# Performance work log

Hardware: AMD Instinct MI355X
Metric: run time of the kernel (lower is better)

The kernel has to match this reference:

```python
import jax, jax.numpy as jnp
import numpy as np

N_GRAPHS = 100
BN_EPS = 1e-5
L = 4


def batch_norm(x, gamma, beta):
    # torch BatchNorm1d in training mode: biased batch statistics over the node dim
    mu = jnp.mean(x, axis=0)
    var = jnp.var(x, axis=0)
    return gamma * (x - mu) * jax.lax.rsqrt(var + BN_EPS) + beta


def setup_inputs() -> dict:
    key = jax.random.key(0)
    ks = jax.random.split(key, 24)
    N, E, IN, H, C = 50000, 600000, 128, 128, 10
    s = 0.05
    inp = {
        "h": jax.random.normal(ks[0], (N, IN), jnp.float32),
        "snorm_n": jax.random.uniform(ks[1], (N, 1), jnp.float32),
        "edge_src": jax.random.randint(ks[2], (E,), 0, N, jnp.int32),
        "edge_dst": jax.random.randint(ks[3], (E,), 0, N, jnp.int32),
        "graph_ids": jnp.sort(jax.random.randint(ks[4], (N,), 0, N_GRAPHS, jnp.int32)),
        # embedding_h
        "emb_W": jax.random.normal(ks[5], (IN, H), jnp.float32) * s,
        "emb_b": jnp.zeros((H,), jnp.float32),
        # per-layer GIN params, stacked over L layers
        "eps": jnp.zeros((L,), jnp.float32),
        "W1": jax.random.normal(ks[6], (L, H, H), jnp.float32) * s,
        "b1": jnp.zeros((L, H), jnp.float32),
        "g1": jnp.ones((L, H), jnp.float32),   # MLP internal BN gamma
        "be1": jnp.zeros((L, H), jnp.float32),  # MLP internal BN beta
        "W2": jax.random.normal(ks[7], (L, H, H), jnp.float32) * s,
        "b2": jnp.zeros((L, H), jnp.float32),
        "ga": jnp.ones((L, H), jnp.float32),    # ApplyNodeFunc BN gamma
        "ba": jnp.zeros((L, H), jnp.float32),
        "gl": jnp.ones((L, H), jnp.float32),    # GINLayer node BN gamma
        "bl": jnp.zeros((L, H), jnp.float32),
        # linears_prediction (L+1 of them)
        "pred_W": jax.random.normal(ks[8], (L + 1, H, C), jnp.float32) * s,
        "pred_b": jnp.zeros((L + 1, C), jnp.float32),
    }
    return inp


def reference(h, snorm_n, edge_src, edge_dst, graph_ids, emb_W, emb_b, eps,
              W1, b1, g1, be1, W2, b2, ga, ba, gl, bl, pred_W, pred_b):
    N = h.shape[0]
    h = h @ emb_W + emb_b  # embedding_h
    hidden_rep = [h]
    for i in range(L):
        h_in = h
        # sum-aggregate neighbor features (irregular gather + scatter-add)
        neigh = jax.ops.segment_sum(h[edge_src], edge_dst, num_segments=N)
        z = (1.0 + eps[i]) * h + neigh
        # ApplyNodeFunc: MLP (lin->BN->relu->lin) then BN then relu
        z = jax.nn.relu(batch_norm(z @ W1[i] + b1[i], g1[i], be1[i]))
        z = z @ W2[i] + b2[i]
        z = jax.nn.relu(batch_norm(z, ga[i], ba[i]))
        z = z * snorm_n                      # graph_norm
        z = batch_norm(z, gl[i], bl[i])      # batch_norm
        z = jax.nn.relu(z)
        h = h_in + z                         # residual (dropout p=0)
        hidden_rep.append(h)
    score = jnp.zeros((N_GRAPHS, pred_W.shape[-1]), h.dtype)
    for i, hr in enumerate(hidden_rep):
        pooled = jax.ops.segment_sum(hr, graph_ids, num_segments=N_GRAPHS)
        score = score + pooled @ pred_W[i] + pred_b[i]
    return score
```

## Files before the change

### kernel.cpp

```cpp
#include <hip/hip_runtime.h>

#define HD __device__ __forceinline__

static constexpr int H = 128;
static constexpr int G = 100;
static constexpr int L = 4;
static constexpr int C = 10;
static constexpr int DEGCAP = 64;

typedef __attribute__((ext_vector_type(8))) short short8;
typedef __attribute__((ext_vector_type(4))) float f32x4;

HD float bf2f(unsigned int u16) {
    return __uint_as_float(u16 << 16);
}
HD unsigned int f2bf(float f) {
    unsigned int u = __float_as_uint(f);
    u += 0x7fffu + ((u >> 16) & 1u);
    return u >> 16;
}

__global__ __launch_bounds__(256) void prep_kernel(
    const float* __restrict__ embW, const float* __restrict__ W1, const float* __restrict__ W2,
    unsigned short* __restrict__ WT, unsigned short* __restrict__ Hb,
    const int* __restrict__ src, const int* __restrict__ dst, int E,
    int* __restrict__ cnt, int* __restrict__ esrc) {
    int b = blockIdx.x;
    if (b < 576) {
        int mat = b >> 6;
        int bx = b & 63;
        if (b == 0 && threadIdx.x < 64)
            ((unsigned int*)Hb)[threadIdx.x] = 0u;
        const float* s = (mat == 0) ? embW
                       : (mat <= L) ? W1 + (size_t)(mat - 1) * H * H
                                    : W2 + (size_t)(mat - 1 - L) * H * H;
        int t = bx * 256 + threadIdx.x;
        int col = t >> 7, k = t & 127;
        WT[(size_t)mat * H * H + col * H + k] = (unsigned short)f2bf(s[(size_t)k * H + col]);
    } else {
        int e = (b - 576) * 256 + threadIdx.x;
        if (e < E) {
            int d = dst[e];
            int pos = atomicAdd(&cnt[d], 1) & (DEGCAP - 1);
            esrc[(size_t)d * DEGCAP + pos] = src[e] + 1;
        }
    }
}

__global__ __launch_bounds__(1024, 2) void aggemm_kernel(
    const unsigned short* __restrict__ HbZ, const int* __restrict__ cnt,
    const int* __restrict__ esrc, const float* __restrict__ eps, int layer,
    const unsigned short* __restrict__ WT, const float* __restrict__ bias,
    unsigned short* __restrict__ outB, int N,
    float* __restrict__ sum_out, float* __restrict__ sq_out) {
    __shared__ unsigned short As[64 * 136];
    int tid = threadIdx.x;
    int w = tid >> 6, lane = tid & 63, q = lane >> 4, m = lane & 15;
    int row0 = blockIdx.x * 64;

    {
        const unsigned int* H2 = (const unsigned int*)HbZ;
        float e1 = 1.0f + eps[layer];
#pragma unroll
        for (int i = 0; i < 4; ++i) {
            int r = w * 4 + i;
            int node = row0 + r;
            unsigned int out = 0;
            if (node < N) {
                unsigned int hv = H2[(size_t)(node + 1) * 64 + lane];
                float ax = e1 * bf2f(hv & 0xffffu);
                float ay = e1 * bf2f(hv >> 16);
                int deg = min(cnt[node], DEGCAP);
                int degPad = min((deg + 15) & ~15, DEGCAP);
                const int* ep = esrc + (size_t)node * DEGCAP;
                for (int j = 0; j < degPad; j += 16) {
                    unsigned int v[16];
#pragma unroll
                    for (int u = 0; u < 16; ++u) v[u] = H2[(size_t)ep[j + u] * 64 + lane];
                    float sx[4] = {0.f, 0.f, 0.f, 0.f}, sy[4] = {0.f, 0.f, 0.f, 0.f};
#pragma unroll
                    for (int u = 0; u < 16; ++u) {
                        sx[u & 3] += bf2f(v[u] & 0xffffu);
                        sy[u & 3] += bf2f(v[u] >> 16);
                    }
                    ax += (sx[0] + sx[1]) + (sx[2] + sx[3]);
                    ay += (sy[0] + sy[1]) + (sy[2] + sy[3]);
                }
                out = f2bf(ax) | (f2bf(ay) << 16);
            }
            *(unsigned int*)&As[r * 136 + lane * 2] = out;
        }
    }
    __syncthreads();

    int mrow = (w >> 2) * 16;
    int colbase = (w & 3) * 32;
    short8 bfrag[2][4];
#pragma unroll
    for (int nt = 0; nt < 2; ++nt) {
        const unsigned short* wc = WT + (size_t)(colbase + nt * 16 + m) * H;
#pragma unroll
        for (int kk = 0; kk < 4; ++kk)
            bfrag[nt][kk] = *(const short8*)&wc[kk * 32 + q * 8];
    }
    f32x4 acc[2] = {(f32x4){0.f, 0.f, 0.f, 0.f}, (f32x4){0.f, 0.f, 0.f, 0.f}};
#pragma unroll
    for (int kk = 0; kk < 4; ++kk) {
        short8 af = *(const short8*)&As[(mrow + m) * 136 + kk * 32 + q * 8];
#pragma unroll
        for (int nt = 0; nt < 2; ++nt)
            acc[nt] = __builtin_amdgcn_mfma_f32_16x16x32_bf16(af, bfrag[nt][kk], acc[nt], 0, 0, 0);
    }

    float bs2[2] = {bias[colbase + m], bias[colbase + 16 + m]};
    float s[2] = {0.f, 0.f}, qq[2] = {0.f, 0.f};
#pragma unroll
    for (int nt = 0; nt < 2; ++nt) {
        int gcol = colbase + nt * 16 + m;
#pragma unroll
        for (int rg = 0; rg < 4; ++rg) {
            int grow = row0 + mrow + q * 4 + rg;
            float v = acc[nt][rg] + bs2[nt];
            if (grow < N) {
                outB[(size_t)grow * H + gcol] = (unsigned short)f2bf(v);
                s[nt] += v;
                qq[nt] += v * v;
            }
        }
    }
#pragma unroll
    for (int nt = 0; nt < 2; ++nt) {
        s[nt] += __shfl_xor(s[nt], 16); s[nt] += __shfl_xor(s[nt], 32);
        qq[nt] += __shfl_xor(qq[nt], 16); qq[nt] += __shfl_xor(qq[nt], 32);
    }
    __syncthreads();
    float* SS = (float*)As;
    float* QQ = SS + 4 * H;
    if (q == 0) {
#pragma unroll
        for (int nt = 0; nt < 2; ++nt) {
            int col = colbase + nt * 16 + m;
            SS[(w >> 2) * H + col] = s[nt];
            QQ[(w >> 2) * H + col] = qq[nt];
        }
    }
    __syncthreads();
    if (tid < H) {
        atomicAdd(&sum_out[tid], SS[tid] + SS[H + tid] + SS[2 * H + tid] + SS[3 * H + tid]);
        atomicAdd(&sq_out[tid], QQ[tid] + QQ[H + tid] + QQ[2 * H + tid] + QQ[3 * H + tid]);
    }
}

template <bool ABF16, bool TRANS, bool STATS, bool POOLF, bool HOFF>
__global__ __launch_bounds__(256, 4) void mgemm_kernel(
    const float* __restrict__ Af, const unsigned short* __restrict__ Ab,
    const unsigned short* __restrict__ WT, const float* __restrict__ bias,
    const float* __restrict__ sum_in, const float* __restrict__ sq_in,
    const float* __restrict__ gam, const float* __restrict__ bet, float invN,
    unsigned short* __restrict__ outB,
    int N, float* __restrict__ sum_out, float* __restrict__ sq_out,
    const int* __restrict__ gids, float* __restrict__ pool) {
    __shared__ unsigned short As[64 * 136];
    __shared__ float cas[H], ccs[H];
    int tid = threadIdx.x;
    int w = tid >> 6, lane = tid & 63, q = lane >> 4, m = lane & 15;
    int row0 = blockIdx.x * 64;
    int colbase = w * 32;

    short8 bfrag[2][4];
#pragma unroll
    for (int nt = 0; nt < 2; ++nt) {
        const unsigned short* wc = WT + (size_t)(colbase + nt * 16 + m) * H;
#pragma unroll
        for (int kk = 0; kk < 4; ++kk)
            bfrag[nt][kk] = *(const short8*)&wc[kk * 32 + q * 8];
    }

    if (TRANS) {
        if (tid < H) {
            float mu = sum_in[tid] * invN;
            float var = sq_in[tid] * invN - mu * mu;
            float inv = rsqrtf(var + 1e-5f);
            float a = gam[tid] * inv;
            cas[tid] = a;
            ccs[tid] = bet[tid] - mu * a;
        }
        __syncthreads();
    }

    {
        int cc = tid & 15, rg = tid >> 4;
        int c0 = cc * 8;
        float a8[8], b8[8];
        if (TRANS) {
#pragma unroll
            for (int j = 0; j < 8; ++j) { a8[j] = cas[c0 + j]; b8[j] = ccs[c0 + j]; }
        }
#pragma unroll
        for (int rr = 0; rr < 4; ++rr) {
            int r = rg * 4 + rr;
            int gr = row0 + r;
            uint4 o = {0u, 0u, 0u, 0u};
            if (ABF16 && !TRANS) {
                if (gr < N) o = *(const uint4*)&Ab[(size_t)gr * H + c0];
            } else {
                float v[8] = {0.f, 0.f, 0.f, 0.f, 0.f, 0.f, 0.f, 0.f};
                if (gr < N) {
                    if (ABF16) {
                        uint4 x = *(const uint4*)&Ab[(size_t)gr * H + c0];
                        v[0] = bf2f(x.x & 0xffffu); v[1] = bf2f(x.x >> 16);
                        v[2] = bf2f(x.y & 0xffffu); v[3] = bf2f(x.y >> 16);
                        v[4] = bf2f(x.z & 0xffffu); v[5] = bf2f(x.z >> 16);
                        v[6] = bf2f(x.w & 0xffffu); v[7] = bf2f(x.w >> 16);
                    } else {
                        float4 x0 = *(const float4*)&Af[(size_t)gr * H + c0];
                        float4 x1 = *(const float4*)&Af[(size_t)gr * H + c0 + 4];
                        v[0] = x0.x; v[1] = x0.y; v[2] = x0.z; v[3] = x0.w;
                        v[4] = x1.x; v[5] = x1.y; v[6] = x1.z; v[7] = x1.w;
                    }
                }
                if (TRANS) {
#pragma unroll
                    for (int j = 0; j < 8; ++j) v[j] = fmaxf(a8[j] * v[j] + b8[j], 0.f);
                }
                o.x = f2bf(v[0]) | (f2bf(v[1]) << 16);
                o.y = f2bf(v[2]) | (f2bf(v[3]) << 16);
                o.z = f2bf(v[4]) | (f2bf(v[5]) << 16);
                o.w = f2bf(v[6]) | (f2bf(v[7]) << 16);
            }
            *(uint4*)&As[r * 136 + c0] = o;
        }
    }
    __syncthreads();

    f32x4 acc[4][2];
#pragma unroll
    for (int mt = 0; mt < 4; ++mt)
#pragma unroll
        for (int nt = 0; nt < 2; ++nt) acc[mt][nt] = (f32x4){0.f, 0.f, 0.f, 0.f};
#pragma unroll
    for (int kk = 0; kk < 4; ++kk) {
        short8 af[4];
#pragma unroll
        for (int mt = 0; mt < 4; ++mt)
            af[mt] = *(const short8*)&As[(mt * 16 + m) * 136 + kk * 32 + q * 8];
#pragma unroll
        for (int mt = 0; mt < 4; ++mt)
#pragma unroll
            for (int nt = 0; nt < 2; ++nt)
                acc[mt][nt] = __builtin_amdgcn_mfma_f32_16x16x32_bf16(
                    af[mt], bfrag[nt][kk], acc[mt][nt], 0, 0, 0);
    }

    float bs2[2] = {bias[colbase + m], bias[colbase + 16 + m]};
    float s[2] = {0.f, 0.f}, qq[2] = {0.f, 0.f};
#pragma unroll
    for (int mt = 0; mt < 4; ++mt)
#pragma unroll
        for (int nt = 0; nt < 2; ++nt) {
            int gcol = colbase + nt * 16 + m;
#pragma unroll
            for (int rg = 0; rg < 4; ++rg) {
                int grow = row0 + mt * 16 + q * 4 + rg;
                float v = acc[mt][nt][rg] + bs2[nt];
                if (grow < N) {
                    outB[(size_t)(HOFF ? grow + 1 : grow) * H + gcol] = (unsigned short)f2bf(v);
                    if (STATS || POOLF) {
                        s[nt] += v;
                        if (STATS) qq[nt] += v * v;
                    }
                }
            }
        }

    if (STATS) {
#pragma unroll
        for (int nt = 0; nt < 2; ++nt) {
            float sv = s[nt], qv = qq[nt];
            sv += __shfl_xor(sv, 16); sv += __shfl_xor(sv, 32);
            qv += __shfl_xor(qv, 16); qv += __shfl_xor(qv, 32);
            if (q == 0) {
                atomicAdd(&sum_out[colbase + nt * 16 + m], sv);
                atomicAdd(&sq_out[colbase + nt * 16 + m], qv);
            }
        }
    }

    if (POOLF) {
        int last = min(row0 + 63, N - 1);
        bool uni = (gids[row0] == gids[last]);
        if (uni) {
            int g = gids[row0];
#pragma unroll
            for (int nt = 0; nt < 2; ++nt) {
                float sv = s[nt];
                sv += __shfl_xor(sv, 16); sv += __shfl_xor(sv, 32);
                if (q == 0) atomicAdd(&pool[g * H + colbase + nt * 16 + m], sv);
            }
        } else {
#pragma unroll
            for (int mt = 0; mt < 4; ++mt)
#pragma unroll
                for (int nt = 0; nt < 2; ++nt)
#pragma unroll
                    for (int rg = 0; rg < 4; ++rg) {
                        int grow = row0 + mt * 16 + q * 4 + rg;
                        if (grow < N) {
                            float v = acc[mt][nt][rg] + bs2[nt];
                            atomicAdd(&pool[gids[grow] * H + colbase + nt * 16 + m], v);
                        }
                    }
        }
    }
}

__global__ __launch_bounds__(256) void statsv_kernel(const unsigned short* __restrict__ UB,
                                                     const float* __restrict__ snorm,
                                                     const float* __restrict__ sum2, const float* __restrict__ sq2,
                                                     const float* __restrict__ ga, const float* __restrict__ ba,
                                                     float invN, int N,
                                                     float* __restrict__ sum3, float* __restrict__ sq3) {
    __shared__ float cas[H], ccs[H];
    int t = threadIdx.x;
    if (t < H) {
        float m = sum2[t] * invN;
        float var = sq2[t] * invN - m * m;
        float inv = rsqrtf(var + 1e-5f);
        float a = ga[t] * inv;
        cas[t] = a;
        ccs[t] = ba[t] - m * a;
    }
    __syncthreads();
    int col2 = t & 63, part = t >> 6;
    int c0 = col2 * 2, c1 = c0 + 1;
    float a0 = cas[c0], b0 = ccs[c0], a1 = cas[c1], b1 = ccs[c1];
    float s0 = 0.f, q0 = 0.f, s1 = 0.f, q1 = 0.f;
    const unsigned int* U2 = (const unsigned int*)UB;
    for (int r = blockIdx.x * 4 + part; r < N; r += gridDim.x * 4) {
        float sn = snorm[r];
        unsigned int v = U2[(size_t)r * 64 + col2];
        float v0 = fmaxf(a0 * bf2f(v & 0xffffu) + b0, 0.f) * sn;
        float v1 = fmaxf(a1 * bf2f(v >> 16) + b1, 0.f) * sn;
        s0 += v0; q0 += v0 * v0;
        s1 += v1; q1 += v1 * v1;
    }
    __shared__ float S[4][H], Q[4][H];
    S[part][c0] = s0; S[part][c1] = s1;
    Q[part][c0] = q0; Q[part][c1] = q1;
    __syncthreads();
    if (t < H) {
        atomicAdd(&sum3[t], S[0][t] + S[1][t] + S[2][t] + S[3][t]);
        atomicAdd(&sq3[t], Q[0][t] + Q[1][t] + Q[2][t] + Q[3][t]);
    }
}

__global__ __launch_bounds__(256) void tail_kernel(unsigned short* __restrict__ HbZ,
                                                   const unsigned short* __restrict__ UB,
                                                   const float* __restrict__ snorm,
                                                   const float* __restrict__ sum2, const float* __restrict__ sq2,
                                                   const float* __restrict__ ga, const float* __restrict__ ba,
                                                   const float* __restrict__ sum3, const float* __restrict__ sq3,
                                                   const float* __restrict__ gl, const float* __restrict__ bl,
                                                   float invN, const int* __restrict__ gids,
                                                   float* __restrict__ pool, int N) {
    __shared__ float ca2[H], cc2[H], ca3[H], cc3[H];
    __shared__ float PS[8][H];
    int t = threadIdx.x;
    if (t < H) {
        float m2 = sum2[t] * invN, v2 = sq2[t] * invN - m2 * m2;
        float i2 = rsqrtf(v2 + 1e-5f), a2 = ga[t] * i2;
        ca2[t] = a2; cc2[t] = ba[t] - m2 * a2;
        float m3 = sum3[t] * invN, v3 = sq3[t] * invN - m3 * m3;
        float i3 = rsqrtf(v3 + 1e-5f), a3 = gl[t] * i3;
        ca3[t] = a3; cc3[t] = bl[t] - m3 * a3;
    }
    __syncthreads();
    int row0 = blockIdx.x * 32;
    int col4 = t & 31, rowg = t >> 5;
    int c0 = col4 * 4;
    float A2[4], B2[4], A3[4], B3[4];
#pragma unroll
    for (int j = 0; j < 4; ++j) {
        A2[j] = ca2[c0 + j]; B2[j] = cc2[c0 + j];
        A3[j] = ca3[c0 + j]; B3[j] = cc3[c0 + j];
    }
    bool uni = (gids[row0] == gids[min(row0 + 31, N - 1)]);
    float p[4] = {0.f, 0.f, 0.f, 0.f};
    const uint2* U4 = (const uint2*)UB;
    uint2* H4 = (uint2*)HbZ;
#pragma unroll
    for (int rr = 0; rr < 4; ++rr) {
        int r = row0 + rowg * 4 + rr;
        if (r < N) {
            float sn = snorm[r];
            uint2 uv = U4[(size_t)r * 32 + col4];
            uint2 hv = H4[(size_t)(r + 1) * 32 + col4];
            float u[4] = {bf2f(uv.x & 0xffffu), bf2f(uv.x >> 16), bf2f(uv.y & 0xffffu), bf2f(uv.y >> 16)};
            float h[4] = {bf2f(hv.x & 0xffffu), bf2f(hv.x >> 16), bf2f(hv.y & 0xffffu), bf2f(hv.y >> 16)};
#pragma unroll
            for (int j = 0; j < 4; ++j) {
                float v = fmaxf(A2[j] * u[j] + B2[j], 0.f) * sn;
                h[j] += fmaxf(A3[j] * v + B3[j], 0.f);
            }
            uint2 hb;
            hb.x = f2bf(h[0]) | (f2bf(h[1]) << 16);
            hb.y = f2bf(h[2]) | (f2bf(h[3]) << 16);
            H4[(size_t)(r + 1) * 32 + col4] = hb;
            if (uni) {
                p[0] += h[0]; p[1] += h[1]; p[2] += h[2]; p[3] += h[3];
            } else {
                int g = gids[r];
#pragma unroll
                for (int j = 0; j < 4; ++j) atomicAdd(&pool[g * H + c0 + j], h[j]);
            }
        }
    }
    if (uni) {
#pragma unroll
        for (int j = 0; j < 4; ++j) PS[rowg][c0 + j] = p[j];
        __syncthreads();
        if (t < H) {
            float s = PS[0][t] + PS[1][t] + PS[2][t] + PS[3][t] +
                      PS[4][t] + PS[5][t] + PS[6][t] + PS[7][t];
            atomicAdd(&pool[gids[row0] * H + t], s);
        }
    }
}

__global__ void final_kernel(const float* __restrict__ pool, const float* __restrict__ pw,
                             const float* __restrict__ pb, float* __restrict__ out) {
    int g = blockIdx.x, t = threadIdx.x;
    __shared__ float p[H];
    float acc = 0.f;
    for (int i = 0; i <= L; ++i) {
        p[t] = pool[(size_t)(i * G + g) * H + t];
        __syncthreads();
        if (t < C) {
            float s = 0.f;
            for (int f = 0; f < H; ++f) s += p[f] * pw[(size_t)(i * H + f) * C + t];
            acc += s + pb[i * C + t];
        }
        __syncthreads();
    }
    if (t < C) out[g * C + t] = acc;
}

extern "C" void kernel_launch(void* const* d_in, const int* in_sizes, int n_in,
                              void* d_out, int out_size, void* d_ws, size_t ws_size,
                              hipStream_t stream) {
    const float* h_in  = (const float*)d_in[0];
    const float* snorm = (const float*)d_in[1];
    const int* esrc_in = (const int*)d_in[2];
    const int* edst_in = (const int*)d_in[3];
    const int* gids    = (const int*)d_in[4];
    const float* embW = (const float*)d_in[5];
    const float* embB = (const float*)d_in[6];
    const float* eps  = (const float*)d_in[7];
    const float* W1   = (const float*)d_in[8];
    const float* b1   = (const float*)d_in[9];
    const float* g1   = (const float*)d_in[10];
    const float* be1  = (const float*)d_in[11];
    const float* W2   = (const float*)d_in[12];
    const float* b2   = (const float*)d_in[13];
    const float* ga   = (const float*)d_in[14];
    const float* ba   = (const float*)d_in[15];
    const float* gl   = (const float*)d_in[16];
    const float* bl   = (const float*)d_in[17];
    const float* predW = (const float*)d_in[18];
    const float* predB = (const float*)d_in[19];

    const int N = in_sizes[0] / H;
    const int E = in_sizes[2];
    const float invN = 1.0f / (float)N;

    float* ws = (float*)d_ws;
    float* POOL = ws;
    float* STATS = POOL + (size_t)(L + 1) * G * H;
    int* CNT = (int*)(STATS + (size_t)L * 6 * H);
    int* ESRC = CNT + N;
    unsigned short* WT = (unsigned short*)(ESRC + (size_t)N * DEGCAP);
    unsigned short* Hb = WT + (size_t)9 * H * H;
    unsigned short* ZB = Hb + (size_t)(N + 1) * H;
    unsigned short* TB = ZB + (size_t)N * H;
    unsigned short* UB = ZB;

    size_t zbytes = ((size_t)(L + 1) * G * H + (size_t)L * 6 * H + N + (size_t)N * DEGCAP) * 4;
    hipMemsetAsync(POOL, 0, zbytes, stream);

    int prep_blocks = 576 + (E + 255) / 256;
    prep_kernel<<<prep_blocks, 256, 0, stream>>>(embW, W1, W2, WT, Hb,
                                                 esrc_in, edst_in, E, CNT, ESRC);

    int gblocks = (N + 63) / 64;
    mgemm_kernel<false, false, false, true, true><<<gblocks, 256, 0, stream>>>(
        h_in, nullptr, WT, embB, nullptr, nullptr, nullptr, nullptr, invN,
        Hb, N, nullptr, nullptr, gids, POOL);

    for (int i = 0; i < L; ++i) {
        float* S1 = STATS + (size_t)i * 6 * H;
        float* Q1 = S1 + H;
        float* S2 = Q1 + H;
        float* Q2 = S2 + H;
        float* S3 = Q2 + H;
        float* Q3 = S3 + H;
        aggemm_kernel<<<gblocks, 1024, 0, stream>>>(
            Hb, CNT, ESRC, eps, i, WT + (size_t)(1 + i) * H * H, b1 + (size_t)i * H,
            TB, N, S1, Q1);
        mgemm_kernel<true, true, true, false, false><<<gblocks, 256, 0, stream>>>(
            nullptr, TB, WT + (size_t)(1 + L + i) * H * H, b2 + (size_t)i * H,
            S1, Q1, g1 + (size_t)i * H, be1 + (size_t)i * H, invN,
            UB, N, S2, Q2, nullptr, nullptr);
        statsv_kernel<<<256, 256, 0, stream>>>(UB, snorm, S2, Q2,
                                               ga + (size_t)i * H, ba + (size_t)i * H, invN, N, S3, Q3);
        tail_kernel<<<(N + 31) / 32, 256, 0, stream>>>(Hb, UB, snorm,
                                                       S2, Q2, ga + (size_t)i * H, ba + (size_t)i * H,
                                                       S3, Q3, gl + (size_t)i * H, bl + (size_t)i * H,
                                                       invN, gids, POOL + (size_t)(i + 1) * G * H, N);
    }
    final_kernel<<<G, H, 0, stream>>>(POOL, predW, predB, (float*)d_out);
}
```

Before: 671.0 us.

## Batch neighbor index loads and interleave two nodes' gathers; parallelize final prediction

The aggregation stage now loads the first 16 edge indices of all four nodes with one coalesced load per wave and broadcasts them with readlane. It issues the gathers for two nodes back to back before reducing, which raises memory-level parallelism on the irregular gather and drops per-edge scalar index loads. The common first chunk is always gathered unconditionally, so low-degree nodes still fetch padded entries. Separately, the final prediction kernel spreads the feature dot products across all 128 threads with a shuffle reduction instead of 10 serial threads.

After: 684.5 us. +2.0%, slower.

```diff
diff --git a/kernel.cpp b/kernel.cpp
--- a/kernel.cpp
+++ b/kernel.cpp
@@ -18,6 +18,17 @@
     unsigned int u = __float_as_uint(f);
     u += 0x7fffu + ((u >> 16) & 1u);
     return u >> 16;
+}
+
+HD void accum16(const unsigned int* v, float& ax, float& ay) {
+    float sx[4] = {0.f, 0.f, 0.f, 0.f}, sy[4] = {0.f, 0.f, 0.f, 0.f};
+#pragma unroll
+    for (int u = 0; u < 16; ++u) {
+        sx[u & 3] += bf2f(v[u] & 0xffffu);
+        sy[u & 3] += bf2f(v[u] >> 16);
+    }
+    ax += (sx[0] + sx[1]) + (sx[2] + sx[3]);
+    ay += (sy[0] + sy[1]) + (sy[2] + sy[3]);
 }
 
 __global__ __launch_bounds__(256) void prep_kernel(
@@ -61,34 +72,65 @@
     {
         const unsigned int* H2 = (const unsigned int*)HbZ;
         float e1 = 1.0f + eps[layer];
+        int nb = row0 + w * 4;
+
+        int esafe = min(nb + (lane >> 4), N - 1);
+        int eperm = esrc[(size_t)esafe * DEGCAP + (lane & 15)];
+
+        int deg[4];
+        unsigned int self[4];
 #pragma unroll
         for (int i = 0; i < 4; ++i) {
-            int r = w * 4 + i;
-            int node = row0 + r;
-            unsigned int out = 0;
-            if (node < N) {
-                unsigned int hv = H2[(size_t)(node + 1) * 64 + lane];
-                float ax = e1 * bf2f(hv & 0xffffu);
-                float ay = e1 * bf2f(hv >> 16);
-                int deg = min(cnt[node], DEGCAP);
-                int degPad = min((deg + 15) & ~15, DEGCAP);
-                const int* ep = esrc + (size_t)node * DEGCAP;
-                for (int j = 0; j < degPad; j += 16) {
-                    unsigned int v[16];
-#pragma unroll
-                    for (int u = 0; u < 16; ++u) v[u] = H2[(size_t)ep[j + u] * 64 + lane];
-                    float sx[4] = {0.f, 0.f, 0.f, 0.f}, sy[4] = {0.f, 0.f, 0.f, 0.f};
-#pragma unroll
-                    for (int u = 0; u < 16; ++u) {
-                        sx[u & 3] += bf2f(v[u] & 0xffffu);
-                        sy[u & 3] += bf2f(v[u] >> 16);
-                    }
-                    ax += (sx[0] + sx[1]) + (sx[2] + sx[3]);
-                    ay += (sy[0] + sy[1]) + (sy[2] + sy[3]);
+            int nd = nb + i;
+            deg[i] = (nd < N) ? min(cnt[nd], DEGCAP) : 0;
+            self[i] = (nd < N) ? H2[(size_t)(nd + 1) * 64 + lane] : 0u;
+        }
+
+#pragma unroll
+        for (int pr = 0; pr < 2; ++pr) {
+            int iA = pr * 2, iB = iA + 1;
+            unsigned int vA[16], vB[16];
+#pragma unroll
+            for (int u = 0; u < 16; ++u) {
+                int a = __builtin_amdgcn_readlane(eperm, iA * 16 + u);
+                vA[u] = H2[(size_t)a * 64 + lane];
+            }
+#pragma unroll
+            for (int u = 0; u < 16; ++u) {
+                int a = __builtin_amdgcn_readlane(eperm, iB * 16 + u);
+                vB[u] = H2[(size_t)a * 64 + lane];
+            }
+            float ax = e1 * bf2f(self[iA] & 0xffffu);
+            float ay = e1 * bf2f(self[iA] >> 16);
+            accum16(vA, ax, ay);
+            if (deg[iA] > 16) {
+                const int* ep = esrc + (size_t)(nb + iA) * DEGCAP;
+                int degPad = min((deg[iA] + 15) & ~15, DEGCAP);
+                for (int j = 16; j < degPad; j += 16) {
+                    unsigned int vv[16];
+#pragma unroll
+                    for (int u = 0; u < 16; ++u) vv[u] = H2[(size_t)ep[j + u] * 64 + lane];
+                    accum16(vv, ax, ay);
                 }
-                out = f2bf(ax) | (f2bf(ay) << 16);
-            }
-            *(unsigned int*)&As[r * 136 + lane * 2] = out;
+            }
+            *(unsigned int*)&As[(w * 4 + iA) * 136 + lane * 2] =
+                (nb + iA < N) ? (f2bf(ax) | (f2bf(ay) << 16)) : 0u;
+
+            float bx = e1 * bf2f(self[iB] & 0xffffu);
+            float by = e1 * bf2f(self[iB] >> 16);
+            accum16(vB, bx, by);
+            if (deg[iB] > 16) {
+                const int* ep = esrc + (size_t)(nb + iB) * DEGCAP;
+                int degPad = min((deg[iB] + 15) & ~15, DEGCAP);
+                for (int j = 16; j < degPad; j += 16) {
+                    unsigned int vv[16];
+#pragma unroll
+                    for (int u = 0; u < 16; ++u) vv[u] = H2[(size_t)ep[j + u] * 64 + lane];
+                    accum16(vv, bx, by);
+                }
+            }
+            *(unsigned int*)&As[(w * 4 + iB) * 136 + lane * 2] =
+                (nb + iB < N) ? (f2bf(bx) | (f2bf(by) << 16)) : 0u;
         }
     }
     __syncthreads();
@@ -427,22 +469,41 @@
     }
 }
 
-__global__ void final_kernel(const float* __restrict__ pool, const float* __restrict__ pw,
-                             const float* __restrict__ pb, float* __restrict__ out) {
+__global__ __launch_bounds__(128) void final_kernel(const float* __restrict__ pool,
+                                                    const float* __restrict__ pw,
+                                                    const float* __restrict__ pb,
+                                                    float* __restrict__ out) {
     int g = blockIdx.x, t = threadIdx.x;
-    __shared__ float p[H];
-    float acc = 0.f;
+    float acc[C];
+#pragma unroll
+    for (int c = 0; c < C; ++c) acc[c] = 0.f;
+#pragma unroll
     for (int i = 0; i <= L; ++i) {
-        p[t] = pool[(size_t)(i * G + g) * H + t];
-        __syncthreads();
-        if (t < C) {
-            float s = 0.f;
-            for (int f = 0; f < H; ++f) s += p[f] * pw[(size_t)(i * H + f) * C + t];
-            acc += s + pb[i * C + t];
-        }
-        __syncthreads();
-    }
-    if (t < C) out[g * C + t] = acc;
+        float p = pool[(size_t)(i * G + g) * H + t];
+        const float* wrow = pw + (size_t)(i * H + t) * C;
+#pragma unroll
+        for (int c = 0; c < C; ++c) acc[c] += p * wrow[c];
+    }
+#pragma unroll
+    for (int c = 0; c < C; ++c) {
+        float v = acc[c];
+        v += __shfl_xor(v, 1);  v += __shfl_xor(v, 2);  v += __shfl_xor(v, 4);
+        v += __shfl_xor(v, 8);  v += __shfl_xor(v, 16); v += __shfl_xor(v, 32);
+        acc[c] = v;
+    }
+    __shared__ float Ws[2][C];
+    if ((t & 63) == 0) {
+        int wv = t >> 6;
+#pragma unroll
+        for (int c = 0; c < C; ++c) Ws[wv][c] = acc[c];
+    }
+    __syncthreads();
+    if (t < C) {
+        float s = Ws[0][t] + Ws[1][t];
+#pragma unroll
+        for (int i = 0; i <= L; ++i) s += pb[i * C + t];
+        out[g * C + t] = s;
+    }
 }
 
 extern "C" void kernel_launch(void* const* d_in, const int* in_sizes, int n_in,
@@ -517,5 +578,5 @@
                                                        S3, Q3, gl + (size_t)i * H, bl + (size_t)i * H,
                                                        invN, gids, POOL + (size_t)(i + 1) * G * H, N);
     }
-    final_kernel<<<G, H, 0, stream>>>(POOL, predW, predB, (float*)d_out);
-}
+    final_kernel<<<G, 128, 0, stream>>>(POOL, predW, predB, (float*)d_out);
+}
```
